# Kernel tuning notes

Hardware: AMD Instinct MI355X
Metric: run time of the kernel (lower is better)

The kernel has to match this reference:

```python
import jax, jax.numpy as jnp
import numpy as np
from jax import lax

K_NEIGH = 10


def setup_inputs() -> dict:
    key = jax.random.key(0)
    k1, k2, k3, k4, k5 = jax.random.split(key, 5)
    bs, C, T = 8, 256, 2048
    x = jax.random.normal(k1, (bs, C, T), dtype=jnp.float32)
    num_frms = jax.random.randint(k2, (bs,), 0, 2048)
    # Conv1d(in=C, out=C, kernel=3, pad=1): weight [out, in, k], bias [out]
    conv_w = jax.random.normal(k3, (C, C, 3), dtype=jnp.float32) * (1.0 / np.sqrt(3 * C))
    conv_b = jnp.zeros((C,), dtype=jnp.float32)
    # Linear(2*C -> C): weight [out, 2*in], bias [out]
    mlp_w = jax.random.normal(k4, (C, 2 * C), dtype=jnp.float32) * (1.0 / np.sqrt(2 * C))
    mlp_b = jax.random.normal(k5, (C,), dtype=jnp.float32) * 0.01
    return {"x": x, "num_frms": num_frms, "conv_w": conv_w, "conv_b": conv_b,
            "mlp_w": mlp_w, "mlp_b": mlp_b}


def _knn_idx(x, k):
    # x: [bs, C, T]; dif[b,i,j] = ||x[b,:,i] - x[b,:,j]||^2 via norm expansion
    sq = jnp.sum(x * x, axis=1)                      # [bs, T]
    gram = jnp.einsum('bci,bcj->bij', x, x)          # [bs, T, T]
    dif = sq[:, :, None] + sq[:, None, :] - 2.0 * gram
    _, idx = lax.top_k(-dif, k)                      # k smallest distances
    return idx                                       # [bs, T, k]


def reference(x, num_frms, conv_w, conv_b, mlp_w, mlp_b):
    bs, C, T = x.shape
    Cout = conv_w.shape[0]
    # temporal conv branch (kernel 3, stride 1, pad 1)
    c_out = lax.conv_general_dilated(
        x, conv_w, window_strides=(1,), padding=((1, 1),),
        dimension_numbers=('NCH', 'OIH', 'NCH')) + conv_b[None, :, None]
    # graph branch ('par': knn on x)
    idx = _knn_idx(x, K_NEIGH)                                   # [bs, T, k]
    idx_flat = (idx + jnp.arange(bs)[:, None, None] * T).reshape(-1, K_NEIGH)
    feat = x.transpose(0, 2, 1).reshape(bs * T, C)               # [N, C]
    feat_neigh = feat[idx_flat]                                  # [N, k, C]
    ctr = feat[:, None, :]                                       # [N, 1, C]
    cat = jnp.concatenate(
        [feat_neigh, jnp.broadcast_to(ctr, feat_neigh.shape)], axis=-1)  # [N,k,2C]
    g = jnp.einsum('nkc,oc->nko', cat, mlp_w) + mlp_b            # [N, k, Cout]
    # cosine edge weight
    num = jnp.einsum('nkc,nc->nk', feat_neigh, feat)
    den = jnp.sqrt(jnp.sum(feat_neigh * feat_neigh, axis=2)) * \
          jnp.sqrt(jnp.sum(feat * feat, axis=1))[:, None]
    w = num / den                                                # [N, k]
    g = g * w[:, :, None]
    g = jnp.max(g, axis=1)                                       # [N, Cout]
    g_out = g.reshape(bs, T, Cout).transpose(0, 2, 1)            # [bs, Cout, T]
    out = jax.nn.relu(c_out + g_out)
    # MaxPool1d(kernel=2, stride=2)
    out = out.reshape(bs, Cout, T // 2, 2).max(axis=-1)
    return out
```

## Files before the change

kernel.cpp:

```cpp
#include <hip/hip_runtime.h>
#include <hip/hip_bf16.h>
#include <cstdint>

#define T_DIM 2048
#define C_DIM 256
#define BS 8
#define NPTS (BS * T_DIM)
#define KNB 10

typedef __bf16 bf16x8 __attribute__((ext_vector_type(8)));
typedef float f32x4 __attribute__((ext_vector_type(4)));

#define AS1 __attribute__((address_space(1)))
#define AS3 __attribute__((address_space(3)))

__device__ __forceinline__ unsigned short f2bf_rn(float f) {
  unsigned u = __float_as_uint(f);
  unsigned r = (u + 0x7FFFu + ((u >> 16) & 1u)) >> 16;
  return (unsigned short)r;
}
__device__ __forceinline__ float bfbits2f(unsigned short h) {
  return __uint_as_float((unsigned)h << 16);
}
__device__ __forceinline__ __bf16 bfbits(unsigned short h) {
  return __builtin_bit_cast(__bf16, h);
}

__device__ __forceinline__ unsigned key_hi(float sqi, float sqj, float gv) {
  float dif = __fmaf_rn(-2.0f, gv, __fadd_rn(sqi, sqj));
  unsigned u = __float_as_uint(dif);
  return (u & 0x80000000u) ? ~u : (u | 0x80000000u);
}

__device__ __forceinline__ void stage_tile(const __bf16* __restrict__ src, size_t row0,
                                           int ld, int k0, __bf16* lds, int w, int l) {
  int kofs = ((l & 7) ^ (l >> 3)) * 8;
  const __bf16* g0 = src + (row0 + (size_t)(l >> 3)) * ld + k0 + kofs;
  __bf16* lbase = lds + (size_t)(w * 4) * 512;
#pragma unroll
  for (int q4 = 0; q4 < 4; ++q4) {
    __builtin_amdgcn_global_load_lds((AS1 void*)(g0 + (size_t)(w * 4 + q4) * 8 * ld),
                                     (AS3 void*)(lbase + q4 * 512), 16, 0, 0);
  }
}

__device__ __forceinline__ void stage_tile_conv(const __bf16* __restrict__ src, int m0,
                                                int k0in, const __bf16* __restrict__ zp,
                                                __bf16* lds, int w, int l) {
  int tap = k0in >> 8;
  int kshift = tap - 1;
  int k0 = k0in & 255;
  int kofs = ((l & 7) ^ (l >> 3)) * 8;
  int mb = m0 & (T_DIM - 1);
#pragma unroll
  for (int q4 = 0; q4 < 4; ++q4) {
    int q = w * 4 + q4;
    int row = q * 8 + (l >> 3);
    int t = mb + row + kshift;
    const __bf16* g = ((unsigned)t < (unsigned)T_DIM)
                          ? (src + (size_t)(m0 + row + kshift) * C_DIM + k0 + kofs)
                          : (zp + kofs);
    __builtin_amdgcn_global_load_lds((AS1 void*)g, (AS3 void*)(lds + q * 512), 16, 0, 0);
  }
}

__device__ __forceinline__ bf16x8 read_frag(const __bf16* lds, int t16, int ks, int l) {
  int row = t16 * 16 + (l & 15);
  int kb = ks * 64 + ((l >> 4) << 4);
  int byte = row * 128 + (kb ^ ((row & 7) << 4));
  return *(const bf16x8*)((const char*)lds + byte);
}

__global__ __launch_bounds__(256) void k_transpose_split(const float* __restrict__ x,
                                                         __bf16* __restrict__ Fh,
                                                         __bf16* __restrict__ Fl) {
  __shared__ float tile[32][33];
  int b = blockIdx.z;
  int t0 = blockIdx.x * 32;
  int c0 = blockIdx.y * 32;
  int tx = threadIdx.x & 31, ty = threadIdx.x >> 5;
  const float* xb = x + (size_t)b * C_DIM * T_DIM;
#pragma unroll
  for (int r = 0; r < 4; ++r) {
    int c = c0 + ty + 8 * r;
    tile[ty + 8 * r][tx] = xb[(size_t)c * T_DIM + t0 + tx];
  }
  __syncthreads();
#pragma unroll
  for (int r = 0; r < 4; ++r) {
    int t = t0 + ty + 8 * r;
    float v = tile[tx][ty + 8 * r];
    unsigned short hb = f2bf_rn(v);
    float lo = v - bfbits2f(hb);
    size_t o = ((size_t)b * T_DIM + t) * C_DIM + c0 + tx;
    Fh[o] = bfbits(hb);
    Fl[o] = bfbits(f2bf_rn(lo));
  }
}

__global__ __launch_bounds__(256) void k_sq(const __bf16* __restrict__ Fh,
                                            const __bf16* __restrict__ Fl,
                                            float* __restrict__ sq) {
  int n = blockIdx.x * 4 + (threadIdx.x >> 6);
  int lane = threadIdx.x & 63;
  ushort4 hv = ((const ushort4*)Fh)[(size_t)n * 64 + lane];
  ushort4 lv = ((const ushort4*)Fl)[(size_t)n * 64 + lane];
  float s = 0.f;
  {
    float v;
    v = bfbits2f(hv.x) + bfbits2f(lv.x); s = fmaf(v, v, s);
    v = bfbits2f(hv.y) + bfbits2f(lv.y); s = fmaf(v, v, s);
    v = bfbits2f(hv.z) + bfbits2f(lv.z); s = fmaf(v, v, s);
    v = bfbits2f(hv.w) + bfbits2f(lv.w); s = fmaf(v, v, s);
  }
#pragma unroll
  for (int d = 1; d < 64; d <<= 1) s += __shfl_xor(s, d, 64);
  if (lane == 0) sq[n] = s;
}

__global__ __launch_bounds__(256, 2) void k_gram_sym(const __bf16* __restrict__ Fh,
                                                     const __bf16* __restrict__ Fl,
                                                     float* __restrict__ gram) {
  __shared__ __align__(16) char smem[65536];
  __bf16* Ah = (__bf16*)smem;
  __bf16* Al = (__bf16*)(smem + 16384);
  __bf16* Bh = (__bf16*)(smem + 32768);
  __bf16* Bl = (__bf16*)(smem + 49152);

  int b = blockIdx.y;
  int ti = blockIdx.x;
  int by = (int)((sqrtf(8.0f * (float)ti + 1.0f) - 1.0f) * 0.5f);
  if ((by + 1) * (by + 2) / 2 <= ti) by++;
  int bx = ti - by * (by + 1) / 2;

  size_t base = (size_t)b * T_DIM;
  int m0 = by * 128, n0 = bx * 128;
  int tid = threadIdx.x, w = tid >> 6, l = tid & 63;
  int wr = w >> 1, wc = w & 1;
  f32x4 acc[4][4];
#pragma unroll
  for (int i = 0; i < 4; ++i)
#pragma unroll
    for (int j = 0; j < 4; ++j) acc[i][j] = {0.f, 0.f, 0.f, 0.f};

  for (int k0 = 0; k0 < C_DIM; k0 += 64) {
    stage_tile(Fh, base + m0, C_DIM, k0, Ah, w, l);
    stage_tile(Fl, base + m0, C_DIM, k0, Al, w, l);
    stage_tile(Fh, base + n0, C_DIM, k0, Bh, w, l);
    stage_tile(Fl, base + n0, C_DIM, k0, Bl, w, l);
    __syncthreads();
#pragma unroll
    for (int ks = 0; ks < 2; ++ks) {
      bf16x8 ah[4], bh[4], x[4];
#pragma unroll
      for (int i = 0; i < 4; ++i) ah[i] = read_frag(Ah, wr * 4 + i, ks, l);
#pragma unroll
      for (int j = 0; j < 4; ++j) bh[j] = read_frag(Bh, wc * 4 + j, ks, l);
#pragma unroll
      for (int i = 0; i < 4; ++i)
#pragma unroll
        for (int j = 0; j < 4; ++j)
          acc[i][j] = __builtin_amdgcn_mfma_f32_16x16x32_bf16(ah[i], bh[j], acc[i][j], 0, 0, 0);
#pragma unroll
      for (int i = 0; i < 4; ++i) x[i] = read_frag(Al, wr * 4 + i, ks, l);
#pragma unroll
      for (int i = 0; i < 4; ++i)
#pragma unroll
        for (int j = 0; j < 4; ++j)
          acc[i][j] = __builtin_amdgcn_mfma_f32_16x16x32_bf16(x[i], bh[j], acc[i][j], 0, 0, 0);
#pragma unroll
      for (int j = 0; j < 4; ++j) x[j] = read_frag(Bl, wc * 4 + j, ks, l);
#pragma unroll
      for (int i = 0; i < 4; ++i)
#pragma unroll
        for (int j = 0; j < 4; ++j)
          acc[i][j] = __builtin_amdgcn_mfma_f32_16x16x32_bf16(ah[i], x[j], acc[i][j], 0, 0, 0);
    }
    __syncthreads();
  }

  float* gout = gram + (size_t)b * T_DIM * T_DIM;
#pragma unroll
  for (int i = 0; i < 4; ++i) {
    int mrow = m0 + wr * 64 + i * 16 + ((l >> 4) << 2);
#pragma unroll
    for (int j = 0; j < 4; ++j) {
      int ncol = n0 + wc * 64 + j * 16 + (l & 15);
      float* cp = gout + (size_t)mrow * T_DIM + ncol;
#pragma unroll
      for (int r = 0; r < 4; ++r) cp[(size_t)r * T_DIM] = acc[i][j][r];
    }
  }

  if (bx != by) {
    float* Tbuf = (float*)smem;
#pragma unroll
    for (int h = 0; h < 2; ++h) {
      __syncthreads();
      if (wc == h) {
#pragma unroll
        for (int j = 0; j < 4; ++j) {
          int cH = j * 16 + (l & 15);
          float* dst = Tbuf + cH * 132 + wr * 64 + ((l >> 4) << 2);
#pragma unroll
          for (int i = 0; i < 4; ++i) *(f32x4*)(dst + i * 16) = acc[i][j];
        }
      }
      __syncthreads();
      int cH = tid >> 5;
      int c4 = (tid & 31) * 4;
#pragma unroll
      for (int p = 0; p < 8; ++p) {
        f32x4 v = *(const f32x4*)(Tbuf + (size_t)(p * 8 + cH) * 132 + c4);
        *(f32x4*)(gout + (size_t)(n0 + h * 64 + p * 8 + cH) * T_DIM + m0 + c4) = v;
      }
    }
  }
}

__global__ __launch_bounds__(256, 2) void k_gemm16(const __bf16* __restrict__ A,
                                                   const __bf16* __restrict__ Bm,
                                                   float* __restrict__ C, int N, int K,
                                                   int conv, const __bf16* __restrict__ zp) {
  __shared__ __bf16 As[128 * 64], Bs[128 * 64];
  int m0 = blockIdx.y * 128, n0 = blockIdx.x * 128;
  int tid = threadIdx.x, w = tid >> 6, l = tid & 63;
  int wr = w >> 1, wc = w & 1;
  f32x4 acc[4][4];
#pragma unroll
  for (int i = 0; i < 4; ++i)
#pragma unroll
    for (int j = 0; j < 4; ++j) acc[i][j] = {0.f, 0.f, 0.f, 0.f};

  for (int k0 = 0; k0 < K; k0 += 64) {
    if (conv)
      stage_tile_conv(A, m0, k0, zp, As, w, l);
    else
      stage_tile(A, (size_t)m0, C_DIM, k0, As, w, l);
    stage_tile(Bm, (size_t)n0, K, k0, Bs, w, l);
    __syncthreads();
#pragma unroll
    for (int ks = 0; ks < 2; ++ks) {
      bf16x8 af[4], bf_[4];
#pragma unroll
      for (int i = 0; i < 4; ++i) af[i] = read_frag(As, wr * 4 + i, ks, l);
#pragma unroll
      for (int j = 0; j < 4; ++j) bf_[j] = read_frag(Bs, wc * 4 + j, ks, l);
#pragma unroll
      for (int i = 0; i < 4; ++i)
#pragma unroll
        for (int j = 0; j < 4; ++j)
          acc[i][j] = __builtin_amdgcn_mfma_f32_16x16x32_bf16(af[i], bf_[j], acc[i][j], 0, 0, 0);
    }
    __syncthreads();
  }
#pragma unroll
  for (int i = 0; i < 4; ++i) {
    int mrow = m0 + wr * 64 + i * 16 + ((l >> 4) << 2);
#pragma unroll
    for (int j = 0; j < 4; ++j) {
      int ncol = n0 + wc * 64 + j * 16 + (l & 15);
      float* cp = C + (size_t)mrow * N + ncol;
#pragma unroll
      for (int r = 0; r < 4; ++r) cp[(size_t)r * N] = acc[i][j][r];
    }
  }
}

__global__ __launch_bounds__(256) void k_topk(const float* __restrict__ gram,
                                              const float* __restrict__ sq,
                                              int* __restrict__ idxo,
                                              float* __restrict__ wo,
                                              int* __restrict__ flags) {
  int lb = blockIdx.y;
  const float* gramb = gram + (size_t)lb * T_DIM * T_DIM;
  const float* sqb = sq + (size_t)lb * T_DIM;
  int* idxb = idxo + (size_t)lb * T_DIM * KNB;
  float* wbp = wo + (size_t)lb * T_DIM * KNB;

  int row = blockIdx.x * 4 + (threadIdx.x >> 6);
  int lane = threadIdx.x & 63;
  float sqi = sqb[row];
  const float* g = gramb + (size_t)row * T_DIM;
  const f32x4* g4 = (const f32x4*)g;
  const f32x4* s4 = (const f32x4*)sqb;

  unsigned long long p0[4], p1[4], p2[4];
#pragma unroll
  for (int q = 0; q < 4; ++q) { p0[q] = ~0ull; p1[q] = ~0ull; p2[q] = ~0ull; }
#pragma unroll 4
  for (int tq = 0; tq < 8; ++tq) {
    int i4 = lane + 64 * tq;
    f32x4 gv = g4[i4];
    f32x4 sv = s4[i4];
    unsigned bj = (unsigned)(i4 * 4);
#pragma unroll
    for (int e = 0; e < 4; ++e) {
      unsigned u = key_hi(sqi, sv[e], gv[e]);
      unsigned long long key = ((unsigned long long)u << 32) | (bj + e);
      unsigned long long t1 = (key > p0[e]) ? key : p0[e];
      p0[e] = (key < p0[e]) ? key : p0[e];
      unsigned long long t2 = (t1 > p1[e]) ? t1 : p1[e];
      p1[e] = (t1 < p1[e]) ? t1 : p1[e];
      p2[e] = (t2 < p2[e]) ? t2 : p2[e];
    }
  }
  unsigned long long m0 = p0[0], m1 = p1[0], m2 = p2[0];
#pragma unroll
  for (int q = 1; q < 4; ++q) {
    unsigned long long k0 = p0[q], k1 = p1[q], k2 = p2[q];
    unsigned long long t1 = (k0 > m0) ? k0 : m0;
    m0 = (k0 < m0) ? k0 : m0;
    unsigned long long t2 = (t1 > m1) ? t1 : m1;
    m1 = (t1 < m1) ? t1 : m1;
    m2 = (t2 < m2) ? t2 : m2;
    unsigned long long t3 = (k1 > m1) ? k1 : m1;
    m1 = (k1 < m1) ? k1 : m1;
    m2 = (t3 < m2) ? t3 : m2;
    m2 = (k2 < m2) ? k2 : m2;
  }
  unsigned long long excl = m2;

  unsigned long long theta = 0;
#pragma unroll
  for (int s = 0; s < KNB; ++s) {
    unsigned long long m = m0;
#pragma unroll
    for (int d = 1; d < 64; d <<= 1) {
      unsigned long long o = __shfl_xor(m, d, 64);
      m = (o < m) ? o : m;
    }
    unsigned long long bal = __ballot(m0 == m);
    int leader = (int)__builtin_ctzll(bal);
    if (lane == leader) { m0 = m1; m1 = ~0ull; }
    if (lane == 0) {
      int j = (int)(unsigned)(m & 0xffffffffull);
      unsigned su = (unsigned)(m >> 32);
      unsigned bits = (su & 0x80000000u) ? (su & 0x7fffffffu) : ~su;
      float dif = __uint_as_float(bits);
      float sqj = sqb[j];
      float num = 0.5f * (sqi + sqj - dif);
      float wv = num / (sqrtf(sqi) * sqrtf(sqj));
      idxb[row * KNB + s] = j;
      wbp[row * KNB + s] = wv;
    }
    theta = m;
  }

#pragma unroll
  for (int d = 1; d < 64; d <<= 1) {
    unsigned long long o = __shfl_xor(excl, d, 64);
    excl = (o < excl) ? o : excl;
  }
  if (excl < theta && lane == 0) flags[(size_t)lb * T_DIM + row] = 1;
}

__global__ __launch_bounds__(256) void k_topk_fix(const float* __restrict__ gram,
                                                  const float* __restrict__ sq,
                                                  const int* __restrict__ flags,
                                                  int* __restrict__ idxo,
                                                  float* __restrict__ wo) {
  int lb = blockIdx.y;
  int row = blockIdx.x * 4 + (threadIdx.x >> 6);
  if (!flags[(size_t)lb * T_DIM + row]) return;
  const float* gramb = gram + (size_t)lb * T_DIM * T_DIM;
  const float* sqb = sq + (size_t)lb * T_DIM;
  int* idxb = idxo + (size_t)lb * T_DIM * KNB;
  float* wbp = wo + (size_t)lb * T_DIM * KNB;
  int lane = threadIdx.x & 63;
  float sqi = sqb[row];
  const float* g = gramb + (size_t)row * T_DIM;

  unsigned long long b0 = ~0ull, b1 = ~0ull, b2 = ~0ull, b3 = ~0ull, b4 = ~0ull,
                     b5 = ~0ull, b6 = ~0ull, b7 = ~0ull, b8 = ~0ull, b9 = ~0ull;
  for (int t = 0; t < 32; ++t) {
    unsigned j = (unsigned)(lane + 64 * t);
    unsigned u = key_hi(sqi, sqb[j], g[j]);
    unsigned long long key = ((unsigned long long)u << 32) | j;
    if (key < b9) {
      b9 = key;
      unsigned long long tt;
      if (b9 < b8) { tt = b8; b8 = b9; b9 = tt; }
      if (b8 < b7) { tt = b7; b7 = b8; b8 = tt; }
      if (b7 < b6) { tt = b6; b6 = b7; b7 = tt; }
      if (b6 < b5) { tt = b5; b5 = b6; b6 = tt; }
      if (b5 < b4) { tt = b4; b4 = b5; b5 = tt; }
      if (b4 < b3) { tt = b3; b3 = b4; b4 = tt; }
      if (b3 < b2) { tt = b2; b2 = b3; b3 = tt; }
      if (b2 < b1) { tt = b1; b1 = b2; b2 = tt; }
      if (b1 < b0) { tt = b0; b0 = b1; b1 = tt; }
    }
  }
#pragma unroll
  for (int s = 0; s < KNB; ++s) {
    unsigned long long m = b0;
#pragma unroll
    for (int d = 1; d < 64; d <<= 1) {
      unsigned long long o = __shfl_xor(m, d, 64);
      m = (o < m) ? o : m;
    }
    unsigned long long bal = __ballot(b0 == m);
    int leader = (int)__builtin_ctzll(bal);
    if (lane == leader) {
      b0 = b1; b1 = b2; b2 = b3; b3 = b4; b4 = b5;
      b5 = b6; b6 = b7; b7 = b8; b8 = b9; b9 = ~0ull;
    }
    if (lane == 0) {
      int j = (int)(unsigned)(m & 0xffffffffull);
      unsigned su = (unsigned)(m >> 32);
      unsigned bits = (su & 0x80000000u) ? (su & 0x7fffffffu) : ~su;
      float dif = __uint_as_float(bits);
      float sqj = sqb[j];
      float num = 0.5f * (sqi + sqj - dif);
      float wv = num / (sqrtf(sqi) * sqrtf(sqj));
      idxb[row * KNB + s] = j;
      wbp[row * KNB + s] = wv;
    }
  }
}

__global__ __launch_bounds__(256) void k_gfinal(const float* __restrict__ mlpout,
                                                const float* __restrict__ mlp_b,
                                                const int* __restrict__ idxo,
                                                const float* __restrict__ wo,
                                                const float* __restrict__ convb,
                                                const float* __restrict__ cb,
                                                float* __restrict__ out) {
  __shared__ float tile[32][33];
  __shared__ int sj[64][KNB];
  __shared__ float sw[64][KNB];
  int b = blockIdx.z, c0 = blockIdx.y * 32, t20 = blockIdx.x * 32;
  int tid = threadIdx.x;
  int nbase = b * T_DIM + t20 * 2;
  for (int e = tid; e < 64 * KNB; e += 256) {
    int ln = e / KNB, k = e - ln * KNB;
    sj[ln][k] = b * T_DIM + idxo[(size_t)(nbase + ln) * KNB + k];
    sw[ln][k] = wo[(size_t)(nbase + ln) * KNB + k];
  }
  __syncthreads();
  int tx = tid & 31, ty = tid >> 5;
  int c = c0 + tx;
  float bias_c = cb[c];
  float mbias = mlp_b[c];
#pragma unroll
  for (int rr = 0; rr < 4; ++rr) {
    int lt2 = ty + 8 * rr;
    float res[2];
#pragma unroll
    for (int s = 0; s < 2; ++s) {
      int ln = 2 * lt2 + s;
      int n = nbase + ln;
      float q = mlpout[(size_t)n * 512 + 256 + c] + mbias;
      float mx = -3.4e38f;
#pragma unroll
      for (int k = 0; k < KNB; ++k) {
        float v = (mlpout[(size_t)sj[ln][k] * 512 + c] + q) * sw[ln][k];
        mx = fmaxf(mx, v);
      }
      float v = convb[(size_t)n * C_DIM + c] + mx + bias_c;
      res[s] = fmaxf(v, 0.f);
    }
    tile[lt2][tx] = fmaxf(res[0], res[1]);
  }
  __syncthreads();
#pragma unroll
  for (int rr = 0; rr < 4; ++rr) {
    int cc = c0 + ty + 8 * rr;
    out[((size_t)b * C_DIM + cc) * (T_DIM / 2) + t20 + tx] = tile[tx][ty + 8 * rr];
  }
}

__global__ void k_repack(const float* __restrict__ cw, const float* __restrict__ mw,
                         __bf16* __restrict__ wk3, __bf16* __restrict__ mlpB,
                         __bf16* __restrict__ zp, int* __restrict__ flags) {
  int i = blockIdx.x * 256 + threadIdx.x;
  if (i < NPTS) flags[i] = 0;
  if (i < 3 * C_DIM * C_DIM) {
    int o = i / 768;
    int rem = i - o * 768;
    int tap = rem >> 8;
    int ii = rem & 255;
    wk3[i] = bfbits(f2bf_rn(cw[(size_t)o * 768 + ii * 3 + tap]));
  } else {
    int m = i - 3 * C_DIM * C_DIM;
    if (m < 512 * 256) {
      int r = m >> 8;
      int col = m & 255;
      mlpB[m] = bfbits(f2bf_rn(mw[(size_t)(r & 255) * 512 + ((r >> 8) << 8) + col]));
    }
  }
  if (blockIdx.x == 0 && threadIdx.x < 128) zp[threadIdx.x] = bfbits(0);
}

extern "C" void kernel_launch(void* const* d_in, const int* in_sizes, int n_in,
                              void* d_out, int out_size, void* d_ws, size_t ws_size,
                              hipStream_t stream) {
  const float* x = (const float*)d_in[0];
  const float* conv_w = (const float*)d_in[2];
  const float* conv_b = (const float*)d_in[3];
  const float* mlp_w = (const float*)d_in[4];
  const float* mlp_b = (const float*)d_in[5];
  float* out = (float*)d_out;

  char* ws = (char*)d_ws;
  size_t off = 0;
  auto alloc = [&](size_t bytes) -> void* {
    void* p = ws + off;
    off += (bytes + 255) & ~(size_t)255;
    return p;
  };
  float* gram = (float*)alloc((size_t)BS * T_DIM * T_DIM * 4);
  __bf16* Fh = (__bf16*)alloc((size_t)NPTS * C_DIM * 2);
  __bf16* Fl = (__bf16*)alloc((size_t)NPTS * C_DIM * 2);
  float* convout = (float*)alloc((size_t)NPTS * C_DIM * 4);
  float* mlpout = (float*)alloc((size_t)NPTS * 512 * 4);
  float* sq = (float*)alloc((size_t)NPTS * 4);
  int* idxb = (int*)alloc((size_t)NPTS * KNB * 4);
  float* wb = (float*)alloc((size_t)NPTS * KNB * 4);
  int* flags = (int*)alloc((size_t)NPTS * 4);
  __bf16* wk3 = (__bf16*)alloc((size_t)3 * C_DIM * C_DIM * 2);
  __bf16* mlpB = (__bf16*)alloc((size_t)512 * 256 * 2);
  __bf16* zp = (__bf16*)alloc(512);

  k_repack<<<dim3(1280), 256, 0, stream>>>(conv_w, mlp_w, wk3, mlpB, zp, flags);
  k_transpose_split<<<dim3(T_DIM / 32, C_DIM / 32, BS), 256, 0, stream>>>(x, Fh, Fl);
  k_sq<<<dim3(NPTS / 4), 256, 0, stream>>>(Fh, Fl, sq);

  k_gram_sym<<<dim3(136, BS), 256, 0, stream>>>(Fh, Fl, gram);
  k_topk<<<dim3(T_DIM / 4, BS), 256, 0, stream>>>(gram, sq, idxb, wb, flags);
  k_topk_fix<<<dim3(T_DIM / 4, BS), 256, 0, stream>>>(gram, sq, flags, idxb, wb);

  k_gemm16<<<dim3(512 / 128, NPTS / 128), 256, 0, stream>>>(Fh, mlpB, mlpout, 512, 256, 0, zp);
  k_gemm16<<<dim3(256 / 128, NPTS / 128), 256, 0, stream>>>(Fh, wk3, convout, 256, 768, 1, zp);

  k_gfinal<<<dim3((T_DIM / 2) / 32, C_DIM / 32, BS), 256, 0, stream>>>(
      mlpout, mlp_b, idxb, wb, convout, conv_b, out);
}
```

Baseline: 187.5 us.

## Merge MLP and conv GEMM launches; split top-k wave reduction into 32-bit passes

The two bf16 GEMM launches (MLP projection and 3-tap conv) become one kernel whose grid has 6 column blocks, with blockIdx.x choosing the operand set. This removes a launch and lets the blocks of both GEMMs share the GPU at once. In top-k, each 64-bit wave-min reduction becomes two 32-bit shuffle reductions, one on the high key bits and one on the index. The per-selection epilogue run by lane 0 is replaced by a parallel write-out where lanes 0-9 each handle one neighbour, which costs a small win[] array in registers.

```diff
diff --git a/kernel.cpp b/kernel.cpp
--- a/kernel.cpp
+++ b/kernel.cpp
@@ -218,12 +218,23 @@
   }
 }
 
-__global__ __launch_bounds__(256, 2) void k_gemm16(const __bf16* __restrict__ A,
-                                                   const __bf16* __restrict__ Bm,
-                                                   float* __restrict__ C, int N, int K,
-                                                   int conv, const __bf16* __restrict__ zp) {
+__global__ __launch_bounds__(256, 2) void k_gemm_fused(const __bf16* __restrict__ Fh,
+                                                       const __bf16* __restrict__ mlpB,
+                                                       const __bf16* __restrict__ wk3,
+                                                       float* __restrict__ mlpout,
+                                                       float* __restrict__ convout,
+                                                       const __bf16* __restrict__ zp) {
   __shared__ __bf16 As[128 * 64], Bs[128 * 64];
-  int m0 = blockIdx.y * 128, n0 = blockIdx.x * 128;
+  int bx = blockIdx.x;
+  const __bf16* Bm;
+  float* C;
+  int N, K, conv, n0;
+  if (bx < 4) {
+    Bm = mlpB; C = mlpout; N = 512; K = 256; conv = 0; n0 = bx * 128;
+  } else {
+    Bm = wk3; C = convout; N = 256; K = 768; conv = 1; n0 = (bx - 4) * 128;
+  }
+  int m0 = blockIdx.y * 128;
   int tid = threadIdx.x, w = tid >> 6, l = tid & 63;
   int wr = w >> 1, wc = w & 1;
   f32x4 acc[4][4];
@@ -234,9 +245,9 @@
 
   for (int k0 = 0; k0 < K; k0 += 64) {
     if (conv)
-      stage_tile_conv(A, m0, k0, zp, As, w, l);
+      stage_tile_conv(Fh, m0, k0, zp, As, w, l);
     else
-      stage_tile(A, (size_t)m0, C_DIM, k0, As, w, l);
+      stage_tile(Fh, (size_t)m0, C_DIM, k0, As, w, l);
     stage_tile(Bm, (size_t)n0, K, k0, Bs, w, l);
     __syncthreads();
 #pragma unroll
@@ -321,30 +332,43 @@
   }
   unsigned long long excl = m2;
 
-  unsigned long long theta = 0;
+  unsigned long long win[KNB];
 #pragma unroll
   for (int s = 0; s < KNB; ++s) {
-    unsigned long long m = m0;
+    unsigned mh = (unsigned)(m0 >> 32);
+    unsigned h = mh;
 #pragma unroll
     for (int d = 1; d < 64; d <<= 1) {
-      unsigned long long o = __shfl_xor(m, d, 64);
-      m = (o < m) ? o : m;
-    }
+      unsigned oh = __shfl_xor(h, d, 64);
+      h = (oh < h) ? oh : h;
+    }
+    unsigned lo = (mh == h) ? (unsigned)m0 : 0xFFFFFFFFu;
+#pragma unroll
+    for (int d = 1; d < 64; d <<= 1) {
+      unsigned ol = __shfl_xor(lo, d, 64);
+      lo = (ol < lo) ? ol : lo;
+    }
+    unsigned long long m = ((unsigned long long)h << 32) | lo;
+    win[s] = m;
     unsigned long long bal = __ballot(m0 == m);
     int leader = (int)__builtin_ctzll(bal);
     if (lane == leader) { m0 = m1; m1 = ~0ull; }
-    if (lane == 0) {
-      int j = (int)(unsigned)(m & 0xffffffffull);
-      unsigned su = (unsigned)(m >> 32);
-      unsigned bits = (su & 0x80000000u) ? (su & 0x7fffffffu) : ~su;
-      float dif = __uint_as_float(bits);
-      float sqj = sqb[j];
-      float num = 0.5f * (sqi + sqj - dif);
-      float wv = num / (sqrtf(sqi) * sqrtf(sqj));
-      idxb[row * KNB + s] = j;
-      wbp[row * KNB + s] = wv;
-    }
-    theta = m;
+  }
+  unsigned long long theta = win[KNB - 1];
+
+  unsigned long long mywin = win[0];
+#pragma unroll
+  for (int s = 1; s < KNB; ++s) mywin = (lane == s) ? win[s] : mywin;
+  if (lane < KNB) {
+    int j = (int)(unsigned)(mywin & 0xffffffffull);
+    unsigned su = (unsigned)(mywin >> 32);
+    unsigned bits = (su & 0x80000000u) ? (su & 0x7fffffffu) : ~su;
+    float dif = __uint_as_float(bits);
+    float sqj = sqb[j];
+    float num = 0.5f * (sqi + sqj - dif);
+    float wv = num / (sqrtf(sqi) * sqrtf(sqj));
+    idxb[row * KNB + lane] = j;
+    wbp[row * KNB + lane] = wv;
   }
 
 #pragma unroll
@@ -530,8 +554,7 @@
   k_topk<<<dim3(T_DIM / 4, BS), 256, 0, stream>>>(gram, sq, idxb, wb, flags);
   k_topk_fix<<<dim3(T_DIM / 4, BS), 256, 0, stream>>>(gram, sq, flags, idxb, wb);
 
-  k_gemm16<<<dim3(512 / 128, NPTS / 128), 256, 0, stream>>>(Fh, mlpB, mlpout, 512, 256, 0, zp);
-  k_gemm16<<<dim3(256 / 128, NPTS / 128), 256, 0, stream>>>(Fh, wk3, convout, 256, 768, 1, zp);
+  k_gemm_fused<<<dim3(6, NPTS / 128), 256, 0, stream>>>(Fh, mlpB, wk3, mlpout, convout, zp);
 
   k_gfinal<<<dim3((T_DIM / 2) / 32, C_DIM / 32, BS), 256, 0, stream>>>(
       mlpout, mlp_b, idxb, wb, convout, conv_b, out);
```

After: 173.0 us. 1.08x faster.
